# Performance work log

Measured on AMD Instinct MI355X. Metric: run time of the kernel, lower is better.

The kernel has to match this reference:

```python
import jax, jax.numpy as jnp
import numpy as np

B, S, D = 2, 2048, 1024
H, Hd = 16, 64
THD = H * Hd  # total_head_dim
LAMBDA_INIT = 0.8
ROPE_BASE = 10000.0
GN_EPS = 1e-5


def _rope_tables(seq_len, head_dim, dtype):
    inv_freq = 1.0 / (ROPE_BASE ** (jnp.arange(0, head_dim, 2, dtype=jnp.float32) / head_dim))
    t = jnp.arange(seq_len, dtype=jnp.float32)
    freqs = jnp.outer(t, inv_freq)                      # (S, Hd/2)
    emb = jnp.concatenate([freqs, freqs], axis=-1)      # (S, Hd)
    return jnp.cos(emb).astype(dtype), jnp.sin(emb).astype(dtype)


def _rotate_half(x):
    x1, x2 = jnp.split(x, 2, axis=-1)
    return jnp.concatenate([-x2, x1], axis=-1)


def _apply_rope(q, k, cos, sin):
    # q, k: (B, H, S, Hd); cos/sin: (S, Hd)
    cos = cos[None, None, :, :]
    sin = sin[None, None, :, :]
    q = q * cos + _rotate_half(q) * sin
    k = k * cos + _rotate_half(k) * sin
    return q, k


def setup_inputs() -> dict:
    key = jax.random.key(0)
    ks = jax.random.split(key, 8)
    s_in = 1.0 / np.sqrt(D)
    s_out = 1.0 / np.sqrt(THD)
    return {
        "x": jax.random.normal(ks[0], (B, S, D), dtype=jnp.float32),
        "Wq": jax.random.normal(ks[1], (D, 2 * THD), dtype=jnp.float32) * s_in,
        "Wk": jax.random.normal(ks[2], (D, 2 * THD), dtype=jnp.float32) * s_in,
        "Wv": jax.random.normal(ks[3], (D, THD), dtype=jnp.float32) * s_in,
        "Wo": jax.random.normal(ks[4], (THD, D), dtype=jnp.float32) * s_out,
        "lambda_q1": jnp.full((H,), LAMBDA_INIT, dtype=jnp.float32),
        "lambda_k1": jnp.full((H,), LAMBDA_INIT, dtype=jnp.float32),
        "lambda_q2": jnp.full((H,), LAMBDA_INIT, dtype=jnp.float32),
        "lambda_k2": jnp.full((H,), LAMBDA_INIT, dtype=jnp.float32),
        "lambda_init": jnp.asarray(LAMBDA_INIT, dtype=jnp.float32),
        "gn_weight": jnp.ones((THD,), dtype=jnp.float32),
        "gn_bias": jnp.zeros((THD,), dtype=jnp.float32),
    }


def reference(x, Wq, Wk, Wv, Wo, lambda_q1, lambda_k1, lambda_q2, lambda_k2,
              lambda_init, gn_weight, gn_bias):
    b, s, _ = x.shape
    scale = Hd ** -0.5

    q = (x @ Wq).reshape(b, s, 2, H, Hd).transpose(0, 2, 3, 1, 4)  # (B,2,H,S,Hd)
    k = (x @ Wk).reshape(b, s, 2, H, Hd).transpose(0, 2, 3, 1, 4)
    v = (x @ Wv).reshape(b, s, H, Hd).transpose(0, 2, 1, 3)        # (B,H,S,Hd)

    q1, q2 = q[:, 0], q[:, 1]
    k1, k2 = k[:, 0], k[:, 1]

    cos, sin = _rope_tables(s, Hd, x.dtype)
    q1, k1 = _apply_rope(q1, k1, cos, sin)
    q2, k2 = _apply_rope(q2, k2, cos, sin)

    attn1 = jax.nn.softmax(jnp.einsum("bhqd,bhkd->bhqk", q1, k1) * scale, axis=-1)
    attn2 = jax.nn.softmax(jnp.einsum("bhqd,bhkd->bhqk", q2, k2) * scale, axis=-1)

    lam1 = jnp.exp(lambda_q1 * lambda_k1).reshape(1, H, 1, 1)
    lam2 = jnp.exp(lambda_q2 * lambda_k2).reshape(1, H, 1, 1)
    lam_full = lam1 - lam2 + lambda_init

    attn_diff = attn1 - lam_full * attn2
    out = jnp.einsum("bhqk,bhkd->bhqd", attn_diff, v)              # (B,H,S,Hd)
    out = out.transpose(0, 2, 1, 3).reshape(b * s, H, Hd)           # (B*S,H,Hd)

    # GroupNorm with num_groups=H over channels THD: normalize each head's Hd
    mean = out.mean(axis=-1, keepdims=True)
    var = out.var(axis=-1, keepdims=True)
    out = (out - mean) * jax.lax.rsqrt(var + GN_EPS)
    out = out * gn_weight.reshape(H, Hd) + gn_bias.reshape(H, Hd)

    out = out.reshape(b, s, THD) * (1.0 - lambda_init)
    return out @ Wo
```

## Files before the change

kernel.cpp:

```cpp
#include <hip/hip_runtime.h>
#include <hip/hip_fp16.h>
#include <math.h>

#define NH     16
#define HD     64
#define S_LEN  2048
#define THD_   1024
#define SCALE_LOG2E 0.18033688011112042f

typedef __fp16 f16x8 __attribute__((ext_vector_type(8)));
typedef __fp16 f16x4 __attribute__((ext_vector_type(4)));
typedef __fp16 f16x2 __attribute__((ext_vector_type(2)));
typedef float  f32x4 __attribute__((ext_vector_type(4)));


__device__ inline void wt_body(const float* __restrict__ W,
                               __half* __restrict__ WT, int id, int nmask,
                               int nshift) {
  int n = id & nmask;
  int k8 = (id >> nshift) * 8;
  int N = nmask + 1;
  f16x8 h;
#pragma unroll
  for (int j = 0; j < 8; ++j)
    h[j] = (__fp16)W[(size_t)(k8 + j) * N + n];
  *(f16x8*)(WT + (size_t)n * 1024 + k8) = h;
}

__global__ __launch_bounds__(256) void prep_kernel(
    const float* __restrict__ Wq, const float* __restrict__ Wk,
    __half* __restrict__ WqT, __half* __restrict__ WkT,
    float2* __restrict__ tab) {
  int bid = blockIdx.x;
  int t = threadIdx.x;
  if (bid < 1024) {
    wt_body(Wq, WqT, bid * 256 + t, 2047, 11);
  } else if (bid < 2048) {
    wt_body(Wk, WkT, (bid - 1024) * 256 + t, 2047, 11);
  } else {
    int id = (bid - 2048) * 256 + t;
    int p = id & 31;
    int s = id >> 5;
    float inv = expf(-0.28782313662425574f * (float)p);
    float sn, cs;
    sincosf((float)s * inv, &sn, &cs);
    tab[id] = make_float2(cs, sn);
  }
}

template <int MODE>
__global__ __launch_bounds__(256) void mfma_gemm(const void* __restrict__ Ap,
                                                 const void* __restrict__ Bp,
                                                 void* __restrict__ Cp,
                                                 const float2* __restrict__ tab) {
  __shared__ __fp16 As[128][72];
  __shared__ __fp16 Bs[64][72];
  const int t = threadIdx.x;
  const int w = t >> 6, lane = t & 63;
  const int quad = lane >> 4, lqi = lane & 15;
  const int wm = w * 32;
  const int n0 = blockIdx.x * 64, m0 = blockIdx.y * 128;

  f32x4 acc[2][4];
#pragma unroll
  for (int mt = 0; mt < 2; ++mt)
#pragma unroll
    for (int nt = 0; nt < 4; ++nt) acc[mt][nt] = (f32x4){0.f, 0.f, 0.f, 0.f};

  const int srow = t >> 3;
  const int sc8 = (t & 7) * 8;
  const int gn_ = t & 63;
  const int gk0 = (t >> 6) * 8;

  for (int k0 = 0; k0 < 1024; k0 += 64) {
    if (k0) __syncthreads();
    if (MODE == 3) {
      const __half* A16 = (const __half*)Ap;
#pragma unroll
      for (int p = 0; p < 4; ++p) {
        int row = srow + 32 * p;
        *(f16x8*)&As[row][sc8] =
            *(const f16x8*)(A16 + (size_t)(m0 + row) * 1024 + k0 + sc8);
      }
    } else {
      const float* A32 = (const float*)Ap;
#pragma unroll
      for (int p = 0; p < 4; ++p) {
        int row = srow + 32 * p;
        const float* src = A32 + (size_t)(m0 + row) * 1024 + k0 + sc8;
        float4 u = *(const float4*)src;
        float4 v = *(const float4*)(src + 4);
        f16x8 h;
        h[0] = (__fp16)u.x; h[1] = (__fp16)u.y;
        h[2] = (__fp16)u.z; h[3] = (__fp16)u.w;
        h[4] = (__fp16)v.x; h[5] = (__fp16)v.y;
        h[6] = (__fp16)v.z; h[7] = (__fp16)v.w;
        *(f16x8*)&As[row][sc8] = h;
      }
    }
    if (MODE == 2) {
      const float* B32 = (const float*)Bp;
#pragma unroll
      for (int p = 0; p < 2; ++p) {
        int kc = gk0 + 32 * p;
        f16x8 h;
#pragma unroll
        for (int j = 0; j < 8; ++j)
          h[j] = (__fp16)B32[(size_t)(k0 + kc + j) * 1024 + n0 + gn_];
        *(f16x8*)&Bs[gn_][kc] = h;
      }
    } else {
      const __half* B16 = (const __half*)Bp;
      if (srow < 32) {
#pragma unroll
        for (int p = 0; p < 2; ++p) {
          int row = srow + 32 * p;
          *(f16x8*)&Bs[row][sc8] =
              *(const f16x8*)(B16 + (size_t)(n0 + row) * 1024 + k0 + sc8);
        }
      }
    }
    __syncthreads();
#pragma unroll
    for (int ks = 0; ks < 2; ++ks) {
      f16x8 af[2], bf[4];
#pragma unroll
      for (int mt = 0; mt < 2; ++mt)
        af[mt] = *(const f16x8*)&As[wm + mt * 16 + lqi][ks * 32 + quad * 8];
#pragma unroll
      for (int nt = 0; nt < 4; ++nt)
        bf[nt] = *(const f16x8*)&Bs[nt * 16 + lqi][ks * 32 + quad * 8];
#pragma unroll
      for (int mt = 0; mt < 2; ++mt)
#pragma unroll
        for (int nt = 0; nt < 4; ++nt)
          acc[mt][nt] = __builtin_amdgcn_mfma_f32_16x16x32_f16(
              af[mt], bf[nt], acc[mt][nt], 0, 0, 0);
    }
  }

  const int b = m0 >> 11;
  const int s0 = (m0 & 2047) + wm + quad * 4;
  if (MODE == 0 || MODE == 1) {
    __half* dst = (__half*)Cp;
    const int comp = n0 >> 10, hh = (n0 >> 6) & 15;
    __half* base = dst + ((size_t)(b * 2 + comp) * NH + hh) * (size_t)S_LEN * HD;
#pragma unroll
    for (int nt = 0; nt < 2; ++nt) {
      int p = nt * 16 + lqi;
#pragma unroll
      for (int mt = 0; mt < 2; ++mt) {
#pragma unroll
        for (int i = 0; i < 4; ++i) {
          int s = s0 + mt * 16 + i;
          float2 cs = tab[s * 32 + p];
          float x1 = acc[mt][nt][i], x2 = acc[mt][nt + 2][i];
          float y1 = x1 * cs.x - x2 * cs.y;
          float y2 = x2 * cs.x + x1 * cs.y;
          if (MODE == 1) { y1 *= SCALE_LOG2E; y2 *= SCALE_LOG2E; }
          base[(size_t)s * HD + p] = __float2half(y1);
          base[(size_t)s * HD + p + 32] = __float2half(y2);
        }
      }
    }
  } else if (MODE == 2) {
    __half* vt = (__half*)Cp;
    const int hh = n0 >> 6;
#pragma unroll
    for (int nt = 0; nt < 4; ++nt) {
      int hd = nt * 16 + lqi;
      __half* base = vt + (((size_t)b * NH + hh) * HD + hd) * S_LEN;
#pragma unroll
      for (int mt = 0; mt < 2; ++mt) {
        f16x4 hv;
#pragma unroll
        for (int i = 0; i < 4; ++i) hv[i] = (__fp16)acc[mt][nt][i];
        *(f16x4*)(base + s0 + mt * 16) = hv;
      }
    }
  } else {
    float* Co = (float*)Cp;
#pragma unroll
    for (int mt = 0; mt < 2; ++mt)
#pragma unroll
      for (int i = 0; i < 4; ++i) {
        int m = m0 + wm + mt * 16 + quad * 4 + i;
#pragma unroll
        for (int nt = 0; nt < 4; ++nt)
          Co[(size_t)m * 1024 + n0 + nt * 16 + lqi] = acc[mt][nt][i];
      }
  }
}

__global__ __launch_bounds__(256, 2) void attn_kernel(
    const __half* __restrict__ q_h, const __half* __restrict__ k_h,
    const __half* __restrict__ vt_h, float* __restrict__ out,
    const float* __restrict__ lq1, const float* __restrict__ lk1,
    const float* __restrict__ lq2, const float* __restrict__ lk2,
    const float* __restrict__ lam_init_p) {
  __shared__ __half Ks[2][16][512];
  __shared__ __half Vs[2][4][64][16];

  const int t = threadIdx.x;
  const int w = t >> 6, lane = t & 63;
  const int quad = lane >> 4, lqi = lane & 15;
  const int qt = blockIdx.x;
  const int bh = blockIdx.y;
  const int b = bh >> 4, h = bh & 15;

  const size_t c1 = ((size_t)(b * 2 + 0) * NH + h) * (size_t)S_LEN * HD;
  const size_t c2 = ((size_t)(b * 2 + 1) * NH + h) * (size_t)S_LEN * HD;
  const size_t vtb = ((size_t)b * NH + h) * (size_t)HD * S_LEN;
  const int q0 = qt * 128 + w * 32;

  f16x8 qf[2][2][2];
#pragma unroll
  for (int nt = 0; nt < 2; ++nt)
#pragma unroll
    for (int ks = 0; ks < 2; ++ks) {
      size_t a = (size_t)(q0 + nt * 16 + lqi) * HD + ks * 32 + quad * 8;
      qf[0][nt][ks] = *(const f16x8*)(q_h + c1 + a);
      qf[1][nt][ks] = *(const f16x8*)(q_h + c2 + a);
    }

  f32x4 O[2][4][2];
#pragma unroll
  for (int s = 0; s < 2; ++s)
#pragma unroll
    for (int hm = 0; hm < 4; ++hm)
#pragma unroll
      for (int nt = 0; nt < 2; ++nt) O[s][hm][nt] = (f32x4){0.f, 0.f, 0.f, 0.f};
  float lsum[2][2] = {{0.f, 0.f}, {0.f, 0.f}};

  auto k_src = [&](int c, int k0) -> const __half* {
    if (c < 16) {
      int str = c >> 3, mt = (c >> 1) & 3, ks = c & 1;
      return k_h + (str ? c2 : c1) + (size_t)(k0 + mt * 16 + lqi) * HD +
             ks * 32 + quad * 8;
    }
    int cc = c - 16, ks2 = cc >> 2, mt = cc & 3;
    return vt_h + vtb + (size_t)(mt * 16 + lqi) * S_LEN + k0 + ks2 * 32 +
           quad * 8;
  };
  auto lds_dst = [&](int c, int buf) -> __half* {
    if (c < 16) return &Ks[buf][c][lane * 8];
    int cc = c - 16, ks2 = cc >> 2, mt = cc & 3;
    int kc = ks2 * 2 + (quad >> 1);
    return &Vs[buf][kc][mt * 16 + lqi][(quad & 1) * 8];
  };

  f16x8 r[6];
#pragma unroll
  for (int ci = 0; ci < 6; ++ci) r[ci] = *(const f16x8*)k_src(w + ci * 4, 0);
#pragma unroll
  for (int ci = 0; ci < 6; ++ci) *(f16x8*)lds_dst(w + ci * 4, 0) = r[ci];
  __syncthreads();

  for (int kt = 0; kt < 32; ++kt) {
    const int cur = kt & 1;
    if (kt < 31) {
#pragma unroll
      for (int ci = 0; ci < 6; ++ci)
        r[ci] = *(const f16x8*)k_src(w + ci * 4, (kt + 1) * 64);
    }

#pragma unroll
    for (int mt = 0; mt < 4; ++mt) {
      f16x4 vf[4];
#pragma unroll
      for (int hm = 0; hm < 4; ++hm)
        vf[hm] = *(const f16x4*)&Vs[cur][mt][hm * 16 + lqi][quad * 4];
#pragma unroll
      for (int str = 0; str < 2; ++str) {
        f16x8 kf0 = *(const f16x8*)&Ks[cur][str * 8 + mt * 2 + 0][lane * 8];
        f16x8 kf1 = *(const f16x8*)&Ks[cur][str * 8 + mt * 2 + 1][lane * 8];
#pragma unroll
        for (int nt = 0; nt < 2; ++nt) {
          f32x4 s = (f32x4){0.f, 0.f, 0.f, 0.f};
          s = __builtin_amdgcn_mfma_f32_16x16x32_f16(kf0, qf[str][nt][0], s,
                                                     0, 0, 0);
          s = __builtin_amdgcn_mfma_f32_16x16x32_f16(kf1, qf[str][nt][1], s,
                                                     0, 0, 0);
          float e0 = __builtin_amdgcn_exp2f(s[0]);
          float e1 = __builtin_amdgcn_exp2f(s[1]);
          float e2 = __builtin_amdgcn_exp2f(s[2]);
          float e3 = __builtin_amdgcn_exp2f(s[3]);
          lsum[str][nt] += (e0 + e1) + (e2 + e3);
          union { f16x4 v; f16x2 h2[2]; } pu;
          pu.h2[0] = __builtin_amdgcn_cvt_pkrtz(e0, e1);
          pu.h2[1] = __builtin_amdgcn_cvt_pkrtz(e2, e3);
#pragma unroll
          for (int hm = 0; hm < 4; ++hm)
            O[str][hm][nt] = __builtin_amdgcn_mfma_f32_16x16x16f16(
                vf[hm], pu.v, O[str][hm][nt], 0, 0, 0);
        }
      }
    }

    if (kt < 31) {
#pragma unroll
      for (int ci = 0; ci < 6; ++ci)
        *(f16x8*)lds_dst(w + ci * 4, cur ^ 1) = r[ci];
      __syncthreads();
    }
  }

  const float lam0 = lam_init_p[0];
  const float lam = expf(lq1[h] * lk1[h]) - expf(lq2[h] * lk2[h]) + lam0;
#pragma unroll
  for (int str = 0; str < 2; ++str)
#pragma unroll
    for (int nt = 0; nt < 2; ++nt) {
      float v = lsum[str][nt];
      v += __shfl_xor(v, 16);
      v += __shfl_xor(v, 32);
      lsum[str][nt] = v;
    }
#pragma unroll
  for (int nt = 0; nt < 2; ++nt) {
    float il1 = 1.f / lsum[0][nt];
    float il2 = lam / lsum[1][nt];
    int q = q0 + nt * 16 + lqi;
#pragma unroll
    for (int hm = 0; hm < 4; ++hm) {
      f32x4 o;
#pragma unroll
      for (int i = 0; i < 4; ++i)
        o[i] = O[0][hm][nt][i] * il1 - O[1][hm][nt][i] * il2;
      *(f32x4*)(out + ((size_t)(b * S_LEN + q)) * THD_ + h * HD + hm * 16 +
                quad * 4) = o;
    }
  }
}

__global__ __launch_bounds__(256) void gn_wt_kernel(
    const float* __restrict__ src, __half* __restrict__ dst,
    const float* __restrict__ gw, const float* __restrict__ gb,
    const float* __restrict__ lam_init_p, const float* __restrict__ Wo,
    __half* __restrict__ WoT) {
  if (blockIdx.x >= 16384) {
    wt_body(Wo, WoT, (blockIdx.x - 16384) * 256 + threadIdx.x, 1023, 10);
    return;
  }
  int g = blockIdx.x * 4 + (threadIdx.x >> 6);
  int lane = threadIdx.x & 63;
  float v = src[(size_t)g * 64 + lane];
  float s = v, sq = v * v;
#pragma unroll
  for (int off = 32; off; off >>= 1) {
    s += __shfl_xor(s, off);
    sq += __shfl_xor(sq, off);
  }
  float mean = s * (1.f / 64.f);
  float var = sq * (1.f / 64.f) - mean * mean;
  float rs = rsqrtf(var + 1e-5f);
  int h = g & 15;
  float w = gw[h * 64 + lane], bb = gb[h * 64 + lane];
  dst[(size_t)g * 64 + lane] =
      __float2half(((v - mean) * rs * w + bb) * (1.f - lam_init_p[0]));
}

extern "C" void kernel_launch(void* const* d_in, const int* in_sizes, int n_in,
                              void* d_out, int out_size, void* d_ws,
                              size_t ws_size, hipStream_t stream) {
  const float* x = (const float*)d_in[0];
  const float* Wq = (const float*)d_in[1];
  const float* Wk = (const float*)d_in[2];
  const float* Wv = (const float*)d_in[3];
  const float* Wo = (const float*)d_in[4];
  const float* lq1 = (const float*)d_in[5];
  const float* lk1 = (const float*)d_in[6];
  const float* lq2 = (const float*)d_in[7];
  const float* lk2 = (const float*)d_in[8];
  const float* lam_init = (const float*)d_in[9];
  const float* gnw = (const float*)d_in[10];
  const float* gnb = (const float*)d_in[11];
  float* out = (float*)d_out;

  __half* q_h = (__half*)d_ws;
  __half* k_h = q_h + 8388608;
  __half* vt_h = k_h + 8388608;
  __half* WqT = k_h;
  __half* WkT = vt_h;
  float2* tab = (float2*)(vt_h + 2097152);
  __half* WoT = q_h;
  __half* gn_h = q_h + 1048576;

  dim3 blk(256);
  prep_kernel<<<2304, blk, 0, stream>>>(Wq, Wk, WqT, WkT, tab);
  mfma_gemm<1><<<dim3(32, 32), blk, 0, stream>>>(x, WqT, q_h, tab);
  mfma_gemm<0><<<dim3(32, 32), blk, 0, stream>>>(x, WkT, k_h, tab);
  mfma_gemm<2><<<dim3(16, 32), blk, 0, stream>>>(x, Wv, vt_h, nullptr);
  attn_kernel<<<dim3(16, 32), blk, 0, stream>>>(q_h, k_h, vt_h, out, lq1, lk1,
                                                lq2, lk2, lam_init);
  gn_wt_kernel<<<16896, blk, 0, stream>>>(out, gn_h, gnw, gnb, lam_init, Wo,
                                          WoT);
  mfma_gemm<3><<<dim3(16, 32), blk, 0, stream>>>(gn_h, WoT, out, nullptr);
}
```

Measured before the change: 363.5 us.

## Use 16x16x32 MFMA for PV product with XOR-swizzled row-major V tile

The P·V accumulation now covers two 16-key score tiles per MFMA, using the K=32 f16 instruction instead of two K=16 instructions, which halves the PV MFMA count. The V tile in shared memory changes to a row-major 64x64 layout with an XOR swizzle on 8-element chunks, so each lane can gather its 8-element fragment as two 4-wide loads without bank conflicts, and global loads of V become row-contiguous. The cost is more live registers for the packed score fragments, which may affect occupancy at the current launch bounds.

```diff
diff --git a/kernel.cpp b/kernel.cpp
--- a/kernel.cpp
+++ b/kernel.cpp
@@ -199,11 +199,12 @@
     const float* __restrict__ lq2, const float* __restrict__ lk2,
     const float* __restrict__ lam_init_p) {
   __shared__ __half Ks[2][16][512];
-  __shared__ __half Vs[2][4][64][16];
+  __shared__ __half Vs[2][64][64];
 
   const int t = threadIdx.x;
   const int w = t >> 6, lane = t & 63;
   const int quad = lane >> 4, lqi = lane & 15;
+  const int r7 = lane & 7;
   const int qt = blockIdx.x;
   const int bh = blockIdx.y;
   const int b = bh >> 4, h = bh & 15;
@@ -238,15 +239,16 @@
       return k_h + (str ? c2 : c1) + (size_t)(k0 + mt * 16 + lqi) * HD +
              ks * 32 + quad * 8;
     }
-    int cc = c - 16, ks2 = cc >> 2, mt = cc & 3;
-    return vt_h + vtb + (size_t)(mt * 16 + lqi) * S_LEN + k0 + ks2 * 32 +
-           quad * 8;
+    int cc = c - 16;
+    return vt_h + vtb + (size_t)(cc * 8 + (lane >> 3)) * S_LEN + k0 +
+           (lane & 7) * 8;
   };
   auto lds_dst = [&](int c, int buf) -> __half* {
     if (c < 16) return &Ks[buf][c][lane * 8];
-    int cc = c - 16, ks2 = cc >> 2, mt = cc & 3;
-    int kc = ks2 * 2 + (quad >> 1);
-    return &Vs[buf][kc][mt * 16 + lqi][(quad & 1) * 8];
+    int cc = c - 16;
+    int row = cc * 8 + (lane >> 3);
+    int col = ((lane & 7) ^ (lane >> 3)) * 8;
+    return &Vs[buf][row][col];
   };
 
   f16x8 r[6];
@@ -265,36 +267,63 @@
     }
 
 #pragma unroll
-    for (int mt = 0; mt < 4; ++mt) {
-      f16x4 vf[4];
+    for (int g = 0; g < 2; ++g) {
+      f16x8 vf[4];
+#pragma unroll
+      for (int hm = 0; hm < 4; ++hm) {
+        const __half* vrow = &Vs[cur][hm * 16 + lqi][0];
+        int s0 = (g * 4 + (quad >> 1)) ^ r7;
+        int s1 = (g * 4 + 2 + (quad >> 1)) ^ r7;
+        union { f16x8 v8; f16x4 v4[2]; } u;
+        u.v4[0] = *(const f16x4*)(vrow + s0 * 8 + (quad & 1) * 4);
+        u.v4[1] = *(const f16x4*)(vrow + s1 * 8 + (quad & 1) * 4);
+        vf[hm] = u.v8;
+      }
+      f16x8 bfrag[2][2];
+#pragma unroll
+      for (int str = 0; str < 2; ++str) {
+        f16x8 kf00 = *(const f16x8*)&Ks[cur][str * 8 + g * 4 + 0][lane * 8];
+        f16x8 kf01 = *(const f16x8*)&Ks[cur][str * 8 + g * 4 + 1][lane * 8];
+        f16x8 kf10 = *(const f16x8*)&Ks[cur][str * 8 + g * 4 + 2][lane * 8];
+        f16x8 kf11 = *(const f16x8*)&Ks[cur][str * 8 + g * 4 + 3][lane * 8];
+#pragma unroll
+        for (int nt = 0; nt < 2; ++nt) {
+          f32x4 sa = (f32x4){0.f, 0.f, 0.f, 0.f};
+          f32x4 sb = (f32x4){0.f, 0.f, 0.f, 0.f};
+          sa = __builtin_amdgcn_mfma_f32_16x16x32_f16(kf00, qf[str][nt][0], sa,
+                                                      0, 0, 0);
+          sa = __builtin_amdgcn_mfma_f32_16x16x32_f16(kf01, qf[str][nt][1], sa,
+                                                      0, 0, 0);
+          sb = __builtin_amdgcn_mfma_f32_16x16x32_f16(kf10, qf[str][nt][0], sb,
+                                                      0, 0, 0);
+          sb = __builtin_amdgcn_mfma_f32_16x16x32_f16(kf11, qf[str][nt][1], sb,
+                                                      0, 0, 0);
+          float ea0 = __builtin_amdgcn_exp2f(sa[0]);
+          float ea1 = __builtin_amdgcn_exp2f(sa[1]);
+          float ea2 = __builtin_amdgcn_exp2f(sa[2]);
+          float ea3 = __builtin_amdgcn_exp2f(sa[3]);
+          float eb0 = __builtin_amdgcn_exp2f(sb[0]);
+          float eb1 = __builtin_amdgcn_exp2f(sb[1]);
+          float eb2 = __builtin_amdgcn_exp2f(sb[2]);
+          float eb3 = __builtin_amdgcn_exp2f(sb[3]);
+          lsum[str][nt] += ((ea0 + ea1) + (ea2 + ea3)) +
+                           ((eb0 + eb1) + (eb2 + eb3));
+          union { f16x8 v; f16x2 h2[4]; } pu;
+          pu.h2[0] = __builtin_amdgcn_cvt_pkrtz(ea0, ea1);
+          pu.h2[1] = __builtin_amdgcn_cvt_pkrtz(ea2, ea3);
+          pu.h2[2] = __builtin_amdgcn_cvt_pkrtz(eb0, eb1);
+          pu.h2[3] = __builtin_amdgcn_cvt_pkrtz(eb2, eb3);
+          bfrag[str][nt] = pu.v;
+        }
+      }
 #pragma unroll
       for (int hm = 0; hm < 4; ++hm)
-        vf[hm] = *(const f16x4*)&Vs[cur][mt][hm * 16 + lqi][quad * 4];
-#pragma unroll
-      for (int str = 0; str < 2; ++str) {
-        f16x8 kf0 = *(const f16x8*)&Ks[cur][str * 8 + mt * 2 + 0][lane * 8];
-        f16x8 kf1 = *(const f16x8*)&Ks[cur][str * 8 + mt * 2 + 1][lane * 8];
-#pragma unroll
-        for (int nt = 0; nt < 2; ++nt) {
-          f32x4 s = (f32x4){0.f, 0.f, 0.f, 0.f};
-          s = __builtin_amdgcn_mfma_f32_16x16x32_f16(kf0, qf[str][nt][0], s,
-                                                     0, 0, 0);
-          s = __builtin_amdgcn_mfma_f32_16x16x32_f16(kf1, qf[str][nt][1], s,
-                                                     0, 0, 0);
-          float e0 = __builtin_amdgcn_exp2f(s[0]);
-          float e1 = __builtin_amdgcn_exp2f(s[1]);
-          float e2 = __builtin_amdgcn_exp2f(s[2]);
-          float e3 = __builtin_amdgcn_exp2f(s[3]);
-          lsum[str][nt] += (e0 + e1) + (e2 + e3);
-          union { f16x4 v; f16x2 h2[2]; } pu;
-          pu.h2[0] = __builtin_amdgcn_cvt_pkrtz(e0, e1);
-          pu.h2[1] = __builtin_amdgcn_cvt_pkrtz(e2, e3);
-#pragma unroll
-          for (int hm = 0; hm < 4; ++hm)
-            O[str][hm][nt] = __builtin_amdgcn_mfma_f32_16x16x16f16(
-                vf[hm], pu.v, O[str][hm][nt], 0, 0, 0);
-        }
-      }
+#pragma unroll
+        for (int str = 0; str < 2; ++str)
+#pragma unroll
+          for (int nt = 0; nt < 2; ++nt)
+            O[str][hm][nt] = __builtin_amdgcn_mfma_f32_16x16x32_f16(
+                vf[hm], bfrag[str][nt], O[str][hm][nt], 0, 0, 0);
     }
 
     if (kt < 31) {
```

Result: faster. 337.2 us (-7.2%).
